# Kernel optimization log

Hardware: AMD Instinct MI355X
Metric: run time of the kernel (lower is better)

The kernel has to match this reference:

```python
import jax, jax.numpy as jnp
import numpy as np

N_NODES = 100000
N_EDGES = 1600000
DIM = 128
HEADS = 8
PHC = DIM // HEADS  # per-head channels = 16


def setup_inputs() -> dict:
    key = jax.random.key(0)
    k1, k2, k3, k4, k5 = jax.random.split(key, 5)
    nodes = jax.random.normal(k1, (N_NODES, DIM), dtype=jnp.float32)
    senders = jax.random.randint(k2, (N_EDGES,), 0, N_NODES, dtype=jnp.int32)
    receivers = jax.random.randint(k3, (N_EDGES,), 0, N_NODES, dtype=jnp.int32)
    # VarianceScaling(fan_avg, uniform) ~ limit = sqrt(3/fan_avg)
    lim_w = np.sqrt(3.0 / DIM)
    W = jax.random.uniform(k4, (DIM, DIM), minval=-lim_w, maxval=lim_w, dtype=jnp.float32)
    b = jnp.zeros((DIM,), dtype=jnp.float32)
    lim_a = np.sqrt(3.0 * 2.0 / (2 * PHC + 1))
    attn_w = jax.random.uniform(k5, (2 * PHC, 1), minval=-lim_a, maxval=lim_a, dtype=jnp.float32)
    attn_b = jnp.zeros((1,), dtype=jnp.float32)
    return {"nodes": nodes, "senders": senders, "receivers": receivers,
            "W": W, "b": b, "attn_w": attn_w, "attn_b": attn_b}


def reference(nodes, senders, receivers, W, b, attn_w, attn_b):
    n = nodes.shape[0]
    # linear transform + split heads: [N, H, PHC]
    nt = (nodes @ W + b).reshape(n, HEADS, PHC)
    sent = nt[senders]      # [E, H, PHC] gather
    recv = nt[receivers]    # [E, H, PHC] gather
    # attention logits: Linear(1) over leaky_relu(concat(q,k)) -> [E, H, 1]
    qk = jax.nn.leaky_relu(jnp.concatenate([sent, recv], axis=-1), negative_slope=0.2)
    logits = qk @ attn_w + attn_b  # [E, H, 1]
    # segment softmax over edges grouped by receiver node
    seg_max = jax.ops.segment_max(logits, receivers, num_segments=n)  # [N, H, 1]
    exp = jnp.exp(logits - seg_max[receivers])
    denom = jax.ops.segment_sum(exp, receivers, num_segments=n)  # [N, H, 1]
    alpha = exp / denom[receivers]
    # weighted scatter-sum of sender features
    out = jax.ops.segment_sum(sent * alpha, receivers, num_segments=n)  # [N, H, PHC]
    return out.reshape(n, -1)  # concat=True -> [N, DIM]
```

## Files before the change

kernel.cpp:

```cpp
#include <hip/hip_runtime.h>

#define DIM 128
#define HEADS 8
#define PHC 16

#define BSHIFT 6
#define BNODES 64
#define CAP 1408
#define NBMAX 1600

typedef __bf16 bf16x4 __attribute__((ext_vector_type(4)));
typedef __bf16 bf16x8 __attribute__((ext_vector_type(8)));
typedef float  f32x4  __attribute__((ext_vector_type(4)));

__device__ inline unsigned short f2bf(float x) {
  unsigned int u = __float_as_uint(x);
  unsigned int r = (u + 0x7FFF + ((u >> 16) & 1)) >> 16;
  return (unsigned short)r;
}

__global__ __launch_bounds__(256) void k_prepw(
    const float* __restrict__ W, __bf16* __restrict__ Wh,
    __bf16* __restrict__ Wl, int* __restrict__ gCursor, int NB) {
  const int tuple = blockIdx.x * 256 + threadIdx.x;
  if (tuple < NB) gCursor[tuple] = 0;
  const int ln = tuple & 15;
  const int lg = (tuple >> 4) & 3;
  const int cg = (tuple >> 6) & 7;
  const int kt = tuple >> 9;
  const int col = (cg << 4) + ln;
  bf16x8 h, l;
#pragma unroll
  for (int e = 0; e < 8; ++e) {
    int k = (kt << 5) + ((e >> 2) << 4) + (lg << 2) + (e & 3);
    float wv = W[k * DIM + col];
    __bf16 hh = (__bf16)wv;
    h[e] = hh;
    l[e] = (__bf16)(wv - (float)hh);
  }
  *(bf16x8*)(Wh + tuple * 8) = h;
  *(bf16x8*)(Wl + tuple * 8) = l;
}

#define GROWS 64

__global__ __launch_bounds__(256, 3) void k_gemm_scatter(
    const float* __restrict__ A, const __bf16* __restrict__ Wh,
    const __bf16* __restrict__ Wl, const float* __restrict__ bias,
    const float* __restrict__ attn_w, unsigned int* __restrict__ nt_t,
    float* __restrict__ s_exp_t, const int* __restrict__ send,
    const int* __restrict__ recv, int* __restrict__ gCursor,
    unsigned int* __restrict__ pairs, int E, int NB, int nScat, int n) {
  __shared__ __align__(16) float smemF[GROWS * DIM];

  if (blockIdx.x < nScat) {
    int* cnt = (int*)smemF;
    int* cur = cnt + NBMAX;
    const int t = threadIdx.x;
    for (int i = t; i < NB; i += 256) cnt[i] = 0;
    __syncthreads();
    const int e0 = blockIdx.x * 8192;
    const int e1 = min(e0 + 8192, E);
    for (int i = e0 + t; i < e1; i += 256)
      atomicAdd(&cnt[recv[i] >> BSHIFT], 1);
    __syncthreads();
    for (int i = t; i < NB; i += 256) {
      int c = cnt[i];
      cur[i] = i * CAP + (c ? atomicAdd(&gCursor[i], c) : 0);
    }
    __syncthreads();
    for (int i = e0 + t; i < e1; i += 256) {
      int r = recv[i];
      int b = r >> BSHIFT;
      int p = atomicAdd(&cur[b], 1);
      if (p - b * CAP < CAP)
        pairs[p] = (unsigned int)send[i] | ((unsigned int)(r & (BNODES - 1)) << 17);
    }
    return;
  }

  __bf16* Ah = (__bf16*)smemF;
  __bf16* Al = Ah + GROWS * DIM;
  const int t    = threadIdx.x;
  const int row0 = (blockIdx.x - nScat) * GROWS;
  const int lane = t & 63;
  const int w    = t >> 6;
  const int lg   = lane >> 4;
  const int ln   = lane & 15;

  float4 av[8];
  {
    const float4* A4 = (const float4*)(A + (size_t)row0 * DIM);
    const int lim = min(GROWS, n - row0) * (DIM / 4);
#pragma unroll
    for (int j = 0; j < 8; ++j) {
      int i = t + j * 256;
      av[j] = (i < lim) ? A4[i] : make_float4(0.f, 0.f, 0.f, 0.f);
    }
  }

#pragma unroll
  for (int j = 0; j < 8; ++j) {
    int i = t + j * 256;
    int r = i >> 5, c4 = i & 31;
    int ktc = c4 >> 3, lgc = c4 & 3, ehi = (c4 >> 2) & 1;
    int unit = (r << 4) + (((ktc << 2) + lgc) ^ (r & 15));
    int ei = (unit << 3) + (ehi << 2);
    float x0 = av[j].x, x1 = av[j].y, x2 = av[j].z, x3 = av[j].w;
    __bf16 h0 = (__bf16)x0, h1 = (__bf16)x1, h2 = (__bf16)x2, h3 = (__bf16)x3;
    bf16x4 hv = {h0, h1, h2, h3};
    bf16x4 lv = {(__bf16)(x0 - (float)h0), (__bf16)(x1 - (float)h1),
                 (__bf16)(x2 - (float)h2), (__bf16)(x3 - (float)h3)};
    *(bf16x4*)(Ah + ei) = hv;
    *(bf16x4*)(Al + ei) = lv;
  }

  f32x4 acc[4][2];
  {
    const float b0 = bias[(w << 5) + ln];
    const float b1 = bias[(w << 5) + 16 + ln];
#pragma unroll
    for (int rt = 0; rt < 4; ++rt) {
      acc[rt][0] = (f32x4){b0, b0, b0, b0};
      acc[rt][1] = (f32x4){b1, b1, b1, b1};
    }
  }
  __syncthreads();

  const int cg0 = w << 1;
#pragma unroll
  for (int kt = 0; kt < 4; ++kt) {
    bf16x8 Bh0, Bl0, Bh1, Bl1;
    {
      int i0 = ((((kt << 3) + cg0) << 2) + lg) * 16 + ln;
      int i1 = ((((kt << 3) + cg0 + 1) << 2) + lg) * 16 + ln;
      Bh0 = *(const bf16x8*)(Wh + (i0 << 3));
      Bl0 = *(const bf16x8*)(Wl + (i0 << 3));
      Bh1 = *(const bf16x8*)(Wh + (i1 << 3));
      Bl1 = *(const bf16x8*)(Wl + (i1 << 3));
    }
    bf16x8 ah[4], al[4];
#pragma unroll
    for (int rt = 0; rt < 4; ++rt) {
      int m = (rt << 4) + ln;
      int u = (m << 4) + (((kt << 2) + lg) ^ (m & 15));
      ah[rt] = *(const bf16x8*)(Ah + (u << 3));
      al[rt] = *(const bf16x8*)(Al + (u << 3));
    }
#pragma unroll
    for (int rt = 0; rt < 4; ++rt) {
      acc[rt][0] = __builtin_amdgcn_mfma_f32_16x16x32_bf16(ah[rt], Bh0, acc[rt][0], 0, 0, 0);
      acc[rt][0] = __builtin_amdgcn_mfma_f32_16x16x32_bf16(ah[rt], Bl0, acc[rt][0], 0, 0, 0);
      acc[rt][0] = __builtin_amdgcn_mfma_f32_16x16x32_bf16(al[rt], Bh0, acc[rt][0], 0, 0, 0);
      acc[rt][1] = __builtin_amdgcn_mfma_f32_16x16x32_bf16(ah[rt], Bh1, acc[rt][1], 0, 0, 0);
      acc[rt][1] = __builtin_amdgcn_mfma_f32_16x16x32_bf16(ah[rt], Bl1, acc[rt][1], 0, 0, 0);
      acc[rt][1] = __builtin_amdgcn_mfma_f32_16x16x32_bf16(al[rt], Bh1, acc[rt][1], 0, 0, 0);
    }
  }

  __syncthreads();

#pragma unroll
  for (int rt = 0; rt < 4; ++rt)
#pragma unroll
    for (int ct = 0; ct < 2; ++ct) {
      int colx = ((w << 5) + (ct << 4) + ln) ^ ((lg & 1) << 4);
#pragma unroll
      for (int r = 0; r < 4; ++r) {
        int rowl = (rt << 4) + (lg << 2) + r;
        smemF[(rowl << 7) + colx] = acc[rt][ct][r];
      }
    }

  {
    const float aw = attn_w[ln];
#pragma unroll
    for (int rt = 0; rt < 4; ++rt)
#pragma unroll
      for (int ct = 0; ct < 2; ++ct) {
        const int head = (w << 1) + ct;
#pragma unroll
        for (int r = 0; r < 4; ++r) {
          float v = acc[rt][ct][r];
          float p = (v > 0.f ? v : 0.2f * v) * aw;
          p += __shfl_xor(p, 1);
          p += __shfl_xor(p, 2);
          p += __shfl_xor(p, 4);
          p += __shfl_xor(p, 8);
          if (ln == 0) {
            int row = row0 + (rt << 4) + (lg << 2) + r;
            if (row < n) s_exp_t[(size_t)head * n + row] = __expf(p);
          }
        }
      }
  }
  __syncthreads();

  {
    const int nrow = min(GROWS, n - row0);
    const int r = t >> 2;
    const int q = t & 3;
    if (r < nrow) {
#pragma unroll
      for (int j = 0; j < 8; ++j) {
        int c4 = (j << 2) + q;
        int c4s = c4 ^ (((r >> 2) & 1) << 2);
        f32x4 v = *(const f32x4*)(smemF + (r << 7) + (c4s << 2));
        unsigned int lo = (unsigned int)f2bf(v[0]) | ((unsigned int)f2bf(v[1]) << 16);
        unsigned int hi = (unsigned int)f2bf(v[2]) | ((unsigned int)f2bf(v[3]) << 16);
        ((uint2*)nt_t)[((size_t)j * n + row0 + r) * 4 + q] = make_uint2(lo, hi);
      }
    }
  }
}

__global__ __launch_bounds__(256) void k_buildcsr(
    const unsigned int* __restrict__ pairs, const int* __restrict__ gCursor,
    int* __restrict__ csr_g, unsigned int* __restrict__ meta_g) {
  __shared__ unsigned int buf[CAP];
  __shared__ int hist[BNODES], curl[BNODES];
  __shared__ unsigned int slotmeta[BNODES];
  const int b = blockIdx.x;
  const int t = threadIdx.x;
  const int base = b * CAP;
  const int bsize = min(gCursor[b], CAP);

  for (int i = t; i < bsize; i += 256) buf[i] = pairs[base + i];
  if (t < BNODES) hist[t] = 0;
  __syncthreads();
  for (int i = t; i < bsize; i += 256)
    atomicAdd(&hist[(buf[i] >> 17) & (BNODES - 1)], 1);
  __syncthreads();
  if (t < 64) {
    int v = hist[t];
    int x = v;
#pragma unroll
    for (int off = 1; off < 64; off <<= 1) {
      int y = __shfl_up(x, off);
      if (t >= off) x += y;
    }
    int e = x - v;
    curl[t] = e;
    int rank = 0;
    for (int j = 0; j < 64; ++j) {
      int dj = hist[j];
      rank += (dj > v) || (dj == v && j < t);
    }
    slotmeta[rank] = ((unsigned int)e << 17) | ((unsigned int)v << 6) |
                     (unsigned int)t;
  }
  __syncthreads();
  if (t < 64) meta_g[(b << 6) + t] = slotmeta[t];
  for (int i = t; i < bsize; i += 256) {
    unsigned int v = buf[i];
    int p = atomicAdd(&curl[(v >> 17) & (BNODES - 1)], 1);
    csr_g[base + p] = (int)(v & 0x1FFFF);
  }
}

__global__ __launch_bounds__(256) void k_agg(
    const int* __restrict__ csr_g, const int* __restrict__ gCursor,
    const unsigned int* __restrict__ meta_g, const unsigned int* __restrict__ nt_t,
    const float* __restrict__ s_exp_t, float* __restrict__ out, int n) {
  __shared__ int csr_l[CAP];
  __shared__ unsigned int smeta[BNODES];
  const int b = blockIdx.x >> 3;
  const int h = blockIdx.x & 7;
  const int t = threadIdx.x;
  const int bsize = min(gCursor[b], CAP);

  for (int i = t; i < bsize; i += 256)
    csr_l[i] = __builtin_nontemporal_load(&csr_g[b * CAP + i]);
  if (t < BNODES) smeta[t] = meta_g[(b << 6) + t];
  __syncthreads();

  const int nl = t >> 2;
  const int q  = t & 3;
  const unsigned int m = smeta[nl];
  const int node = (b << BSHIFT) + (int)(m & 63);
  const int deg  = (int)((m >> 6) & 0x7FF);
  const int eoff = (int)(m >> 17);
  const uint2* nt2 = (const uint2*)nt_t;
  const float* sp = s_exp_t + (size_t)h * n;
  const size_t pb4 = (size_t)h * n * 4;

  f32x4 a = {0.f, 0.f, 0.f, 0.f};
  float den = 0.f;
  for (int j = 0; j < deg; j += 4) {
    bool ok1 = (j + 1) < deg, ok2 = (j + 2) < deg, ok3 = (j + 3) < deg;
    int s0 = csr_l[eoff + j];
    int s1 = csr_l[ok1 ? (eoff + j + 1) : eoff];
    int s2 = csr_l[ok2 ? (eoff + j + 2) : eoff];
    int s3 = csr_l[ok3 ? (eoff + j + 3) : eoff];
    float w0 = sp[s0];
    float w1 = ok1 ? sp[s1] : 0.f;
    float w2 = ok2 ? sp[s2] : 0.f;
    float w3 = ok3 ? sp[s3] : 0.f;
    uint2 q0 = nt2[pb4 + s0 * 4 + q];
    uint2 q1 = nt2[pb4 + s1 * 4 + q];
    uint2 q2 = nt2[pb4 + s2 * 4 + q];
    uint2 q3 = nt2[pb4 + s3 * 4 + q];
    den += (w0 + w1) + (w2 + w3);
    a.x = fmaf(w0, __uint_as_float(q0.x << 16),
          fmaf(w1, __uint_as_float(q1.x << 16),
          fmaf(w2, __uint_as_float(q2.x << 16),
          fmaf(w3, __uint_as_float(q3.x << 16), a.x))));
    a.y = fmaf(w0, __uint_as_float(q0.x & 0xFFFF0000u),
          fmaf(w1, __uint_as_float(q1.x & 0xFFFF0000u),
          fmaf(w2, __uint_as_float(q2.x & 0xFFFF0000u),
          fmaf(w3, __uint_as_float(q3.x & 0xFFFF0000u), a.y))));
    a.z = fmaf(w0, __uint_as_float(q0.y << 16),
          fmaf(w1, __uint_as_float(q1.y << 16),
          fmaf(w2, __uint_as_float(q2.y << 16),
          fmaf(w3, __uint_as_float(q3.y << 16), a.z))));
    a.w = fmaf(w0, __uint_as_float(q0.y & 0xFFFF0000u),
          fmaf(w1, __uint_as_float(q1.y & 0xFFFF0000u),
          fmaf(w2, __uint_as_float(q2.y & 0xFFFF0000u),
          fmaf(w3, __uint_as_float(q3.y & 0xFFFF0000u), a.w))));
  }
  if (node < n) {
    const float inv = (deg > 0) ? 1.0f / den : 0.f;
    f32x4 o = {a.x * inv, a.y * inv, a.z * inv, a.w * inv};
    __builtin_nontemporal_store(
        o, (f32x4*)out + (size_t)node * 32 + (h << 2) + q);
  }
}

extern "C" void kernel_launch(void* const* d_in, const int* in_sizes, int n_in,
                              void* d_out, int out_size, void* d_ws, size_t ws_size,
                              hipStream_t stream) {
  const float* nodes   = (const float*)d_in[0];
  const int*   senders = (const int*)d_in[1];
  const int*   recvs   = (const int*)d_in[2];
  const float* W       = (const float*)d_in[3];
  const float* bias    = (const float*)d_in[4];
  const float* attn_w  = (const float*)d_in[5];

  const int n = in_sizes[0] / DIM;
  const int E = in_sizes[1];
  const int NB = (n + BNODES - 1) >> BSHIFT;

  char* w = (char*)d_ws;
  auto align256 = [](size_t x) { return (x + 255) & ~(size_t)255; };
  size_t off = 0;
  unsigned int* nt_t = (unsigned int*)(w + off); off += align256((size_t)n * DIM * 2);
  float* s_exp_t = (float*)(w + off); off += align256((size_t)n * HEADS * 4);
  unsigned int* pairs = (unsigned int*)(w + off); off += align256((size_t)NB * CAP * 4);
  int* csr_g     = (int*)(w + off);   off += align256((size_t)NB * CAP * 4);
  unsigned int* meta_g = (unsigned int*)(w + off); off += align256((size_t)NB * 64 * 4);
  int* gCursor   = (int*)(w + off);   off += align256((size_t)NB * 4);
  __bf16* Wh     = (__bf16*)(w + off); off += align256((size_t)2048 * 8 * 2);
  __bf16* Wl     = (__bf16*)(w + off); off += align256((size_t)2048 * 8 * 2);
  (void)ws_size;

  k_prepw<<<8, 256, 0, stream>>>(W, Wh, Wl, gCursor, NB);
  const int nScat = (E + 8191) / 8192;
  const int ngemm = (n + GROWS - 1) / GROWS;
  k_gemm_scatter<<<nScat + ngemm, 256, 0, stream>>>(
      nodes, Wh, Wl, bias, attn_w, nt_t, s_exp_t,
      senders, recvs, gCursor, pairs, E, NB, nScat, n);
  k_buildcsr<<<NB, 256, 0, stream>>>(pairs, gCursor, csr_g, meta_g);
  k_agg<<<NB * 8, 256, 0, stream>>>(csr_g, gCursor, meta_g, nt_t, s_exp_t,
                                    (float*)d_out, n);
}
```

Measured before the change: 305.4 us.

## Store node features and scores in head-pair layout; aggregate two heads per block

The GEMM epilogue now writes transformed features and exp-scores interleaved in head pairs, giving 64-byte rows per sender per head pair instead of 32-byte rows per head. The aggregation kernel launches half as many blocks. Each block covers two heads, with 8 lanes per node, and loops twice to cover its 64 nodes. The aim is wider, better-used gathered memory segments and half as many reloads of the CSR into shared memory. In exchange, each thread does more serial work and there is less parallelism per block.

```diff
diff --git a/kernel.cpp b/kernel.cpp
--- a/kernel.cpp
+++ b/kernel.cpp
@@ -47,8 +47,8 @@
 __global__ __launch_bounds__(256, 3) void k_gemm_scatter(
     const float* __restrict__ A, const __bf16* __restrict__ Wh,
     const __bf16* __restrict__ Wl, const float* __restrict__ bias,
-    const float* __restrict__ attn_w, unsigned int* __restrict__ nt_t,
-    float* __restrict__ s_exp_t, const int* __restrict__ send,
+    const float* __restrict__ attn_w, unsigned int* __restrict__ nt_hp,
+    float* __restrict__ s_exp_hp, const int* __restrict__ send,
     const int* __restrict__ recv, int* __restrict__ gCursor,
     unsigned int* __restrict__ pairs, int E, int NB, int nScat, int n) {
   __shared__ __align__(16) float smemF[GROWS * DIM];
@@ -178,7 +178,6 @@
     for (int rt = 0; rt < 4; ++rt)
 #pragma unroll
       for (int ct = 0; ct < 2; ++ct) {
-        const int head = (w << 1) + ct;
 #pragma unroll
         for (int r = 0; r < 4; ++r) {
           float v = acc[rt][ct][r];
@@ -189,7 +188,7 @@
           p += __shfl_xor(p, 8);
           if (ln == 0) {
             int row = row0 + (rt << 4) + (lg << 2) + r;
-            if (row < n) s_exp_t[(size_t)head * n + row] = __expf(p);
+            if (row < n) s_exp_hp[((size_t)w * n + row) * 2 + ct] = __expf(p);
           }
         }
       }
@@ -208,7 +207,8 @@
         f32x4 v = *(const f32x4*)(smemF + (r << 7) + (c4s << 2));
         unsigned int lo = (unsigned int)f2bf(v[0]) | ((unsigned int)f2bf(v[1]) << 16);
         unsigned int hi = (unsigned int)f2bf(v[2]) | ((unsigned int)f2bf(v[3]) << 16);
-        ((uint2*)nt_t)[((size_t)j * n + row0 + r) * 4 + q] = make_uint2(lo, hi);
+        ((uint2*)nt_hp)[((size_t)(j >> 1) * n + row0 + r) * 8 + (j & 1) * 4 + q] =
+            make_uint2(lo, hi);
       }
     }
   }
@@ -260,12 +260,12 @@
 
 __global__ __launch_bounds__(256) void k_agg(
     const int* __restrict__ csr_g, const int* __restrict__ gCursor,
-    const unsigned int* __restrict__ meta_g, const unsigned int* __restrict__ nt_t,
-    const float* __restrict__ s_exp_t, float* __restrict__ out, int n) {
+    const unsigned int* __restrict__ meta_g, const unsigned int* __restrict__ nt_hp,
+    const float* __restrict__ s_exp_hp, float* __restrict__ out, int n) {
   __shared__ int csr_l[CAP];
   __shared__ unsigned int smeta[BNODES];
-  const int b = blockIdx.x >> 3;
-  const int h = blockIdx.x & 7;
+  const int b  = blockIdx.x >> 2;
+  const int hp = blockIdx.x & 3;
   const int t = threadIdx.x;
   const int bsize = min(gCursor[b], CAP);
 
@@ -274,55 +274,59 @@
   if (t < BNODES) smeta[t] = meta_g[(b << 6) + t];
   __syncthreads();
 
-  const int nl = t >> 2;
-  const int q  = t & 3;
-  const unsigned int m = smeta[nl];
-  const int node = (b << BSHIFT) + (int)(m & 63);
-  const int deg  = (int)((m >> 6) & 0x7FF);
-  const int eoff = (int)(m >> 17);
-  const uint2* nt2 = (const uint2*)nt_t;
-  const float* sp = s_exp_t + (size_t)h * n;
-  const size_t pb4 = (size_t)h * n * 4;
-
-  f32x4 a = {0.f, 0.f, 0.f, 0.f};
-  float den = 0.f;
-  for (int j = 0; j < deg; j += 4) {
-    bool ok1 = (j + 1) < deg, ok2 = (j + 2) < deg, ok3 = (j + 3) < deg;
-    int s0 = csr_l[eoff + j];
-    int s1 = csr_l[ok1 ? (eoff + j + 1) : eoff];
-    int s2 = csr_l[ok2 ? (eoff + j + 2) : eoff];
-    int s3 = csr_l[ok3 ? (eoff + j + 3) : eoff];
-    float w0 = sp[s0];
-    float w1 = ok1 ? sp[s1] : 0.f;
-    float w2 = ok2 ? sp[s2] : 0.f;
-    float w3 = ok3 ? sp[s3] : 0.f;
-    uint2 q0 = nt2[pb4 + s0 * 4 + q];
-    uint2 q1 = nt2[pb4 + s1 * 4 + q];
-    uint2 q2 = nt2[pb4 + s2 * 4 + q];
-    uint2 q3 = nt2[pb4 + s3 * 4 + q];
-    den += (w0 + w1) + (w2 + w3);
-    a.x = fmaf(w0, __uint_as_float(q0.x << 16),
-          fmaf(w1, __uint_as_float(q1.x << 16),
-          fmaf(w2, __uint_as_float(q2.x << 16),
-          fmaf(w3, __uint_as_float(q3.x << 16), a.x))));
-    a.y = fmaf(w0, __uint_as_float(q0.x & 0xFFFF0000u),
-          fmaf(w1, __uint_as_float(q1.x & 0xFFFF0000u),
-          fmaf(w2, __uint_as_float(q2.x & 0xFFFF0000u),
-          fmaf(w3, __uint_as_float(q3.x & 0xFFFF0000u), a.y))));
-    a.z = fmaf(w0, __uint_as_float(q0.y << 16),
-          fmaf(w1, __uint_as_float(q1.y << 16),
-          fmaf(w2, __uint_as_float(q2.y << 16),
-          fmaf(w3, __uint_as_float(q3.y << 16), a.z))));
-    a.w = fmaf(w0, __uint_as_float(q0.y & 0xFFFF0000u),
-          fmaf(w1, __uint_as_float(q1.y & 0xFFFF0000u),
-          fmaf(w2, __uint_as_float(q2.y & 0xFFFF0000u),
-          fmaf(w3, __uint_as_float(q3.y & 0xFFFF0000u), a.w))));
-  }
-  if (node < n) {
-    const float inv = (deg > 0) ? 1.0f / den : 0.f;
-    f32x4 o = {a.x * inv, a.y * inv, a.z * inv, a.w * inv};
-    __builtin_nontemporal_store(
-        o, (f32x4*)out + (size_t)node * 32 + (h << 2) + q);
+  const int lane8 = t & 7;
+  const int par   = lane8 >> 2;
+  const uint2* nt2 = (const uint2*)nt_hp;
+  const size_t pb8 = (size_t)hp * n * 8;
+  const float* spp = s_exp_hp + (size_t)hp * n * 2;
+
+#pragma unroll 1
+  for (int pi = 0; pi < 2; ++pi) {
+    const int nl = (t >> 3) + (pi << 5);
+    const unsigned int m = smeta[nl];
+    const int node = (b << BSHIFT) + (int)(m & 63);
+    const int deg  = (int)((m >> 6) & 0x7FF);
+    const int eoff = (int)(m >> 17);
+    f32x4 a = {0.f, 0.f, 0.f, 0.f};
+    float den = 0.f;
+    for (int j = 0; j < deg; j += 4) {
+      bool ok1 = (j + 1) < deg, ok2 = (j + 2) < deg, ok3 = (j + 3) < deg;
+      int s0 = csr_l[eoff + j];
+      int s1 = csr_l[ok1 ? (eoff + j + 1) : eoff];
+      int s2 = csr_l[ok2 ? (eoff + j + 2) : eoff];
+      int s3 = csr_l[ok3 ? (eoff + j + 3) : eoff];
+      float w0 = spp[s0 * 2 + par];
+      float w1 = ok1 ? spp[s1 * 2 + par] : 0.f;
+      float w2 = ok2 ? spp[s2 * 2 + par] : 0.f;
+      float w3 = ok3 ? spp[s3 * 2 + par] : 0.f;
+      uint2 q0 = nt2[pb8 + s0 * 8 + lane8];
+      uint2 q1 = nt2[pb8 + s1 * 8 + lane8];
+      uint2 q2 = nt2[pb8 + s2 * 8 + lane8];
+      uint2 q3 = nt2[pb8 + s3 * 8 + lane8];
+      den += (w0 + w1) + (w2 + w3);
+      a.x = fmaf(w0, __uint_as_float(q0.x << 16),
+            fmaf(w1, __uint_as_float(q1.x << 16),
+            fmaf(w2, __uint_as_float(q2.x << 16),
+            fmaf(w3, __uint_as_float(q3.x << 16), a.x))));
+      a.y = fmaf(w0, __uint_as_float(q0.x & 0xFFFF0000u),
+            fmaf(w1, __uint_as_float(q1.x & 0xFFFF0000u),
+            fmaf(w2, __uint_as_float(q2.x & 0xFFFF0000u),
+            fmaf(w3, __uint_as_float(q3.x & 0xFFFF0000u), a.y))));
+      a.z = fmaf(w0, __uint_as_float(q0.y << 16),
+            fmaf(w1, __uint_as_float(q1.y << 16),
+            fmaf(w2, __uint_as_float(q2.y << 16),
+            fmaf(w3, __uint_as_float(q3.y << 16), a.z))));
+      a.w = fmaf(w0, __uint_as_float(q0.y & 0xFFFF0000u),
+            fmaf(w1, __uint_as_float(q1.y & 0xFFFF0000u),
+            fmaf(w2, __uint_as_float(q2.y & 0xFFFF0000u),
+            fmaf(w3, __uint_as_float(q3.y & 0xFFFF0000u), a.w))));
+    }
+    if (node < n) {
+      const float inv = (deg > 0) ? 1.0f / den : 0.f;
+      f32x4 o = {a.x * inv, a.y * inv, a.z * inv, a.w * inv};
+      __builtin_nontemporal_store(
+          o, (f32x4*)out + (size_t)node * 32 + (hp << 3) + lane8);
+    }
   }
 }
 
@@ -343,8 +347,8 @@
   char* w = (char*)d_ws;
   auto align256 = [](size_t x) { return (x + 255) & ~(size_t)255; };
   size_t off = 0;
-  unsigned int* nt_t = (unsigned int*)(w + off); off += align256((size_t)n * DIM * 2);
-  float* s_exp_t = (float*)(w + off); off += align256((size_t)n * HEADS * 4);
+  unsigned int* nt_hp = (unsigned int*)(w + off); off += align256((size_t)n * DIM * 2);
+  float* s_exp_hp = (float*)(w + off); off += align256((size_t)n * HEADS * 4);
   unsigned int* pairs = (unsigned int*)(w + off); off += align256((size_t)NB * CAP * 4);
   int* csr_g     = (int*)(w + off);   off += align256((size_t)NB * CAP * 4);
   unsigned int* meta_g = (unsigned int*)(w + off); off += align256((size_t)NB * 64 * 4);
@@ -357,9 +361,9 @@
   const int nScat = (E + 8191) / 8192;
   const int ngemm = (n + GROWS - 1) / GROWS;
   k_gemm_scatter<<<nScat + ngemm, 256, 0, stream>>>(
-      nodes, Wh, Wl, bias, attn_w, nt_t, s_exp_t,
+      nodes, Wh, Wl, bias, attn_w, nt_hp, s_exp_hp,
       senders, recvs, gCursor, pairs, E, NB, nScat, n);
   k_buildcsr<<<NB, 256, 0, stream>>>(pairs, gCursor, csr_g, meta_g);
-  k_agg<<<NB * 8, 256, 0, stream>>>(csr_g, gCursor, meta_g, nt_t, s_exp_t,
+  k_agg<<<NB * 4, 256, 0, stream>>>(csr_g, gCursor, meta_g, nt_hp, s_exp_hp,
                                     (float*)d_out, n);
 }
```

Result: faster. 261.9 us (-14.2%).
